# Kernel optimization log

Measured on AMD Instinct MI355X. Metric: run time of the kernel, lower is better.

## Reference

```python
import jax, jax.numpy as jnp
import numpy as np
from functools import partial

ALPHA = 0.1
THETA = 0.5
N_NODES = 100000
N_EDGES = 3200000


def _gcn_norm(edge_index, num_nodes):
    # add self loops, compute symmetric normalization D^-1/2 (A+I) D^-1/2
    loops = jnp.arange(num_nodes, dtype=edge_index.dtype)
    src = jnp.concatenate([edge_index[0], loops])
    dst = jnp.concatenate([edge_index[1], loops])
    deg = jax.ops.segment_sum(jnp.ones_like(dst, dtype=jnp.float32), dst,
                              num_segments=num_nodes)
    dinv = jnp.where(deg > 0, jax.lax.rsqrt(deg), 0.0)
    norm = dinv[src] * dinv[dst]  # [E+N]
    return src, dst, norm


def _propagate(h, src, dst, norm, num_nodes):
    # out[i] = sum_{e: dst[e]=i} norm[e] * h[src[e]]
    msg = h[src] * norm[:, None]
    return jax.ops.segment_sum(msg, dst, num_segments=num_nodes)


def setup_inputs() -> dict:
    key = jax.random.key(0)
    ks = jax.random.split(key, 7)
    H, Fin, Fout, L = 256, 512, 64, 8
    x = jax.random.normal(ks[0], (N_NODES, Fin), dtype=jnp.float32)
    edge_index = jax.random.randint(ks[1], (2, N_EDGES), 0, N_NODES, dtype=jnp.int64)
    s = 1.0 / np.sqrt(Fin)
    W0 = jax.random.normal(ks[2], (Fin, H), dtype=jnp.float32) * s
    b0 = jax.random.normal(ks[3], (H,), dtype=jnp.float32) * 0.01
    Ws = jax.random.normal(ks[4], (L, H, H), dtype=jnp.float32) / np.sqrt(H)
    Wc = jax.random.normal(ks[5], (H, Fout), dtype=jnp.float32) / np.sqrt(H)
    bc = jax.random.normal(ks[6], (Fout,), dtype=jnp.float32) * 0.01
    return {"x": x, "edge_index": edge_index, "W0": W0, "b0": b0,
            "Ws": Ws, "Wc": Wc, "bc": bc}


def reference(x, edge_index, W0, b0, Ws, Wc, bc):
    num_nodes = x.shape[0]
    src, dst, norm = _gcn_norm(edge_index, num_nodes)
    # initial projection (dropout is identity in eval mode)
    x0 = jax.nn.relu(x @ W0 + b0)  # [N, H]
    h = x0
    layer_num = Ws.shape[0]
    for i in range(layer_num):
        beta = float(np.log(THETA / (i + 1) + 1.0))
        agg = _propagate(h, src, dst, norm, num_nodes)          # Ahat @ h
        z = (1.0 - ALPHA) * agg + ALPHA * x0                    # initial residual
        h = jax.nn.relu((1.0 - beta) * z + beta * (z @ Ws[i]))  # identity mapping
    embedding = h
    logits = embedding @ Wc + bc
    soft_label = jax.nn.softmax(logits, axis=1)
    hard_label = jnp.argmax(soft_label, axis=1)
    return logits, embedding, soft_label, hard_label
```

## Files before the change

kernel.cpp:

```cpp
#include <hip/hip_runtime.h>
#include <hip/hip_bf16.h>
#include <math.h>

#define NN   100000
#define FIN  512
#define HH   256
#define FOUT 64

typedef __attribute__((ext_vector_type(8))) short s16x8;
typedef __attribute__((ext_vector_type(4))) float f32x4;

__global__ void k_count(const int* __restrict__ dst, int* __restrict__ cnt, int E) {
    int i = blockIdx.x * 256 + threadIdx.x;
    if (i < E) atomicAdd(&cnt[dst[i]], 1);
}

__global__ void k_block_sums(const int* __restrict__ cnt, int* __restrict__ partial, int n) {
    __shared__ int red[256];
    int base = blockIdx.x * 1024;
    int t = threadIdx.x;
    int s = 0;
#pragma unroll
    for (int i = 0; i < 4; i++) { int idx = base + t * 4 + i; if (idx < n) s += cnt[idx]; }
    red[t] = s; __syncthreads();
    for (int off = 128; off > 0; off >>= 1) {
        if (t < off) red[t] += red[t + off];
        __syncthreads();
    }
    if (t == 0) partial[blockIdx.x] = red[0];
}

__global__ void k_scan_partials(int* partial, int nb, int* row_ptr, int n) {
    if (threadIdx.x == 0) {
        int run = 0;
        for (int i = 0; i < nb; i++) { int v = partial[i]; partial[i] = run; run += v; }
        row_ptr[n] = run;
    }
}

__global__ void k_write_rowptr(const int* __restrict__ cnt, const int* __restrict__ partial,
                               int* __restrict__ row_ptr, int* __restrict__ cur, int n) {
    __shared__ int sc[256];
    int base = blockIdx.x * 1024;
    int t = threadIdx.x;
    int v[4]; int s = 0;
#pragma unroll
    for (int i = 0; i < 4; i++) { int idx = base + t * 4 + i; v[i] = (idx < n) ? cnt[idx] : 0; s += v[i]; }
    sc[t] = s; __syncthreads();
    for (int off = 1; off < 256; off <<= 1) {
        int add = (t >= off) ? sc[t - off] : 0;
        __syncthreads();
        sc[t] += add;
        __syncthreads();
    }
    int run = partial[blockIdx.x] + sc[t] - s;
#pragma unroll
    for (int i = 0; i < 4; i++) {
        int idx = base + t * 4 + i;
        if (idx < n) { row_ptr[idx] = run; cur[idx] = run; run += v[i]; }
    }
}

__global__ void k_dinv(const int* __restrict__ cnt, float* __restrict__ dinv, int n) {
    int i = blockIdx.x * 256 + threadIdx.x;
    if (i < n) dinv[i] = 1.0f / sqrtf((float)(cnt[i] + 1));
}

__global__ void k_scatter(const int* __restrict__ src, const int* __restrict__ dst,
                          const float* __restrict__ dinv, int* __restrict__ cur,
                          int* __restrict__ src_sorted, float* __restrict__ norm_sorted, int E) {
    int i = blockIdx.x * 256 + threadIdx.x;
    if (i < E) {
        int s = src[i], d = dst[i];
        int p = atomicAdd(&cur[d], 1);
        src_sorted[p] = s;
        norm_sorted[p] = dinv[s] * dinv[d];
    }
}

__device__ __forceinline__ short f2bf_rn(float f) {
    unsigned b = __float_as_uint(f);
    unsigned r = b + 0x7FFFu + ((b >> 16) & 1u);
    return (short)(r >> 16);
}
__device__ __forceinline__ float bf2f(short h) {
    return __uint_as_float(((unsigned)(unsigned short)h) << 16);
}
__device__ __forceinline__ void split_bf16(float f, short& hi, short& lo) {
    hi = f2bf_rn(f);
    lo = f2bf_rn(f - bf2f(hi));
}

__global__ void k_wprep(const float* __restrict__ W, short* __restrict__ whi,
                        short* __restrict__ wlo, int K) {
    int t = blockIdx.x * 256 + threadIdx.x;
    int total = K * HH / 8;
    if (t >= total) return;
    int colin = t & 15, g = (t >> 4) & 3, nt = (t >> 6) & 15, kt = t >> 10;
    int col = nt * 16 + colin, kb = kt * 32 + g * 8;
    s16x8 h8, l8;
#pragma unroll
    for (int j = 0; j < 8; j++) {
        float f = W[(size_t)(kb + j) * HH + col];
        short h, l; split_bf16(f, h, l);
        h8[j] = h; l8[j] = l;
    }
    *(s16x8*)&whi[(size_t)t * 8] = h8;
    *(s16x8*)&wlo[(size_t)t * 8] = l8;
}

__global__ void k_wprep_all(const float* __restrict__ Ws, short* __restrict__ whi,
                            short* __restrict__ wlo, int L) {
    int t = blockIdx.x * 256 + threadIdx.x;
    const int per = HH * HH / 8;
    if (t >= L * per) return;
    int layer = t / per;
    int tl = t - layer * per;
    float beta = (float)log(0.5 / (layer + 1) + 1.0);
    const float* W = Ws + (size_t)layer * HH * HH;
    int colin = tl & 15, g = (tl >> 4) & 3, nt = (tl >> 6) & 15, kt = tl >> 10;
    int col = nt * 16 + colin, kb = kt * 32 + g * 8;
    s16x8 h8, l8;
#pragma unroll
    for (int j = 0; j < 8; j++) {
        float f = beta * W[(size_t)(kb + j) * HH + col];
        if ((kb + j) == col) f += 1.0f - beta;
        short h, l; split_bf16(f, h, l);
        h8[j] = h; l8[j] = l;
    }
    *(s16x8*)&whi[(size_t)t * 8] = h8;
    *(s16x8*)&wlo[(size_t)t * 8] = l8;
}

__global__ __launch_bounds__(512, 4) void k_gemm0(
    const float* __restrict__ A, const short* __restrict__ Whi, const short* __restrict__ Wlo,
    const float* __restrict__ bias, float* __restrict__ C, int M) {
    __shared__ short As_hi[2][2048];
    __shared__ short As_lo[2][2048];
    int tid = threadIdx.x, lane = tid & 63, wid = tid >> 6;
    int wm = wid >> 2, wn = wid & 3;
    int bm = blockIdx.x * 64;
    int st_row = tid >> 2, st_g = tid & 3;
    int st_cphys = ((st_row & 15) ^ ((st_g & 1) << 2)) + 16 * st_g + 64 * (st_row >> 4);
    const float* st_ap = A + (size_t)(bm + st_row) * FIN + st_g * 8;
    bool st_ok = (tid < 256) && (bm + st_row) < M;
    int fr_g = lane >> 4, fr_r = lane & 15;
    int fr_base = (fr_r ^ ((fr_g & 1) << 2)) + 16 * fr_g;
    int c0 = (fr_base + 64 * (wm * 2 + 0)) * 8;
    int c1 = (fr_base + 64 * (wm * 2 + 1)) * 8;
    int lane_off = fr_g * 16 + fr_r;
    f32x4 acc[2][4] = {};
    f32x4 v0 = {0.f, 0.f, 0.f, 0.f}, v1 = v0, n0 = v0, n1 = v0;
    if (st_ok) { v0 = *(const f32x4*)(st_ap); v1 = *(const f32x4*)(st_ap + 4); }
    for (int kt = 0; kt < FIN / 32; kt++) {
        int buf = kt & 1;
        if (tid < 256) {
            s16x8 h8, l8;
            float fv[8] = {v0.x, v0.y, v0.z, v0.w, v1.x, v1.y, v1.z, v1.w};
#pragma unroll
            for (int j = 0; j < 8; j++) { short hh, ll; split_bf16(fv[j], hh, ll); h8[j] = hh; l8[j] = ll; }
            *(s16x8*)&As_hi[buf][st_cphys * 8] = h8;
            *(s16x8*)&As_lo[buf][st_cphys * 8] = l8;
            if (kt + 1 < FIN / 32 && st_ok) {
                int k0n = (kt + 1) * 32;
                n0 = *(const f32x4*)(st_ap + k0n);
                n1 = *(const f32x4*)(st_ap + k0n + 4);
            }
        }
        __syncthreads();
        s16x8 ah0 = *(const s16x8*)&As_hi[buf][c0], al0 = *(const s16x8*)&As_lo[buf][c0];
        s16x8 ah1 = *(const s16x8*)&As_hi[buf][c1], al1 = *(const s16x8*)&As_lo[buf][c1];
        size_t btile = (size_t)kt * 1024 + (size_t)(wn * 4) * 64;
#pragma unroll
        for (int ct = 0; ct < 4; ct++) {
            s16x8 bh = *(const s16x8*)&Whi[(btile + ct * 64 + lane_off) * 8];
            s16x8 bl = *(const s16x8*)&Wlo[(btile + ct * 64 + lane_off) * 8];
            acc[0][ct] = __builtin_amdgcn_mfma_f32_16x16x32_bf16(ah0, bh, acc[0][ct], 0, 0, 0);
            acc[0][ct] = __builtin_amdgcn_mfma_f32_16x16x32_bf16(al0, bh, acc[0][ct], 0, 0, 0);
            acc[0][ct] = __builtin_amdgcn_mfma_f32_16x16x32_bf16(ah0, bl, acc[0][ct], 0, 0, 0);
            acc[1][ct] = __builtin_amdgcn_mfma_f32_16x16x32_bf16(ah1, bh, acc[1][ct], 0, 0, 0);
            acc[1][ct] = __builtin_amdgcn_mfma_f32_16x16x32_bf16(al1, bh, acc[1][ct], 0, 0, 0);
            acc[1][ct] = __builtin_amdgcn_mfma_f32_16x16x32_bf16(ah1, bl, acc[1][ct], 0, 0, 0);
        }
        v0 = n0; v1 = n1;
        if (kt + 1 < FIN / 32) __syncthreads();
    }
    int rsub = (lane >> 4) * 4, csub = lane & 15;
#pragma unroll
    for (int rt = 0; rt < 2; rt++)
#pragma unroll
        for (int ct = 0; ct < 4; ct++) {
            int col = wn * 64 + ct * 16 + csub;
            int r0 = bm + wm * 32 + rt * 16 + rsub;
#pragma unroll
            for (int reg = 0; reg < 4; reg++) {
                int row = r0 + reg;
                if (row < M) {
                    float o = fmaxf(acc[rt][ct][reg] + bias[col], 0.f);
                    C[(size_t)(col >> 7) * ((size_t)M * 128) + (size_t)row * 128 + (col & 127)] = o;
                }
            }
        }
}

__global__ __launch_bounds__(256) void k_prop(
    const float* __restrict__ hc, const float* __restrict__ x0c,
    const int* __restrict__ row_ptr, const int* __restrict__ src_sorted,
    const float* __restrict__ norm_sorted, const float* __restrict__ dinv,
    float* __restrict__ zc, int M) {
    int wid = threadIdx.x >> 6, lane = threadIdx.x & 63;
    int node = blockIdx.x * 4 + wid;
    if (node >= M) return;
    int slot = lane >> 5, f4 = (lane & 31) * 4;
    int e0 = __builtin_amdgcn_readfirstlane(row_ptr[node]);
    int e1 = __builtin_amdgcn_readfirstlane(row_ptr[node + 1]);
    f32x4 acc = {0.f, 0.f, 0.f, 0.f};
    int e = e0 + slot;
    for (; e + 2 < e1; e += 4) {
        int s0 = src_sorted[e];     float w0 = norm_sorted[e];
        int s1 = src_sorted[e + 2]; float w1 = norm_sorted[e + 2];
        f32x4 v0 = *(const f32x4*)&hc[(size_t)s0 * 128 + f4];
        f32x4 v1 = *(const f32x4*)&hc[(size_t)s1 * 128 + f4];
        acc += w0 * v0 + w1 * v1;
    }
    if (e < e1) {
        int s0 = src_sorted[e]; float w0 = norm_sorted[e];
        acc += w0 * (*(const f32x4*)&hc[(size_t)s0 * 128 + f4]);
    }
#pragma unroll
    for (int c = 0; c < 4; c++) acc[c] += __shfl_xor(acc[c], 32);
    float di = dinv[node], sw = di * di;
    size_t base = (size_t)node * 128 + f4;
    f32x4 hrow = *(const f32x4*)&hc[base];
    f32x4 xv = *(const f32x4*)&x0c[base];
    f32x4 z = 0.9f * (acc + sw * hrow) + 0.1f * xv;
    if (slot == 0) *(f32x4*)&zc[base] = z;
}

__global__ __launch_bounds__(512, 4) void k_mgemm_z(
    const float* __restrict__ Zc, const short* __restrict__ Whi, const short* __restrict__ Wlo,
    float* __restrict__ C, int M, int rowmajor) {
    __shared__ short As_hi[2][2048];
    __shared__ short As_lo[2][2048];
    int tid = threadIdx.x, lane = tid & 63, wid = tid >> 6;
    int wm = wid >> 2, wn = wid & 3;
    int bm = blockIdx.x * 64;
    size_t CS = (size_t)M * 128;
    int st_row = tid >> 2, st_g = tid & 3;
    bool st_ok = (tid < 256) && (bm + st_row) < M;
    int st_cphys = ((st_row & 15) ^ ((st_g & 1) << 2)) + 16 * st_g + 64 * (st_row >> 4);
    int fr_g = lane >> 4, fr_r = lane & 15;
    int fr_base = (fr_r ^ ((fr_g & 1) << 2)) + 16 * fr_g;
    int c0 = (fr_base + 64 * (wm * 2 + 0)) * 8;
    int c1 = (fr_base + 64 * (wm * 2 + 1)) * 8;
    int lane_off = fr_g * 16 + fr_r;
    f32x4 acc[2][4] = {};
    auto zslab = [&](int kt) {
        int k0 = kt * 32;
        return Zc + (size_t)(k0 >> 7) * CS + (size_t)(bm + st_row) * 128 + (k0 & 127) + st_g * 8;
    };
    f32x4 v0 = {0.f, 0.f, 0.f, 0.f}, v1 = v0, n0 = v0, n1 = v0;
    if (st_ok) { const float* zp = zslab(0); v0 = *(const f32x4*)zp; v1 = *(const f32x4*)(zp + 4); }
    for (int kt = 0; kt < 8; kt++) {
        int buf = kt & 1;
        if (tid < 256) {
            s16x8 h8, l8;
            float fv[8] = {v0.x, v0.y, v0.z, v0.w, v1.x, v1.y, v1.z, v1.w};
#pragma unroll
            for (int j = 0; j < 8; j++) { short hh, ll; split_bf16(fv[j], hh, ll); h8[j] = hh; l8[j] = ll; }
            *(s16x8*)&As_hi[buf][st_cphys * 8] = h8;
            *(s16x8*)&As_lo[buf][st_cphys * 8] = l8;
            if (kt + 1 < 8 && st_ok) {
                const float* zp = zslab(kt + 1);
                n0 = *(const f32x4*)zp; n1 = *(const f32x4*)(zp + 4);
            }
        }
        __syncthreads();
        s16x8 ah0 = *(const s16x8*)&As_hi[buf][c0], al0 = *(const s16x8*)&As_lo[buf][c0];
        s16x8 ah1 = *(const s16x8*)&As_hi[buf][c1], al1 = *(const s16x8*)&As_lo[buf][c1];
        size_t btile = (size_t)kt * 1024 + (size_t)(wn * 4) * 64;
#pragma unroll
        for (int ct = 0; ct < 4; ct++) {
            s16x8 bh = *(const s16x8*)&Whi[(btile + ct * 64 + lane_off) * 8];
            s16x8 bl = *(const s16x8*)&Wlo[(btile + ct * 64 + lane_off) * 8];
            acc[0][ct] = __builtin_amdgcn_mfma_f32_16x16x32_bf16(ah0, bh, acc[0][ct], 0, 0, 0);
            acc[0][ct] = __builtin_amdgcn_mfma_f32_16x16x32_bf16(al0, bh, acc[0][ct], 0, 0, 0);
            acc[0][ct] = __builtin_amdgcn_mfma_f32_16x16x32_bf16(ah0, bl, acc[0][ct], 0, 0, 0);
            acc[1][ct] = __builtin_amdgcn_mfma_f32_16x16x32_bf16(ah1, bh, acc[1][ct], 0, 0, 0);
            acc[1][ct] = __builtin_amdgcn_mfma_f32_16x16x32_bf16(al1, bh, acc[1][ct], 0, 0, 0);
            acc[1][ct] = __builtin_amdgcn_mfma_f32_16x16x32_bf16(ah1, bl, acc[1][ct], 0, 0, 0);
        }
        v0 = n0; v1 = n1;
        if (kt + 1 < 8) __syncthreads();
    }
    int rsub = (lane >> 4) * 4, csub = lane & 15;
#pragma unroll
    for (int rt = 0; rt < 2; rt++)
#pragma unroll
        for (int ct = 0; ct < 4; ct++) {
            int col = wn * 64 + ct * 16 + csub;
            int r0 = bm + wm * 32 + rt * 16 + rsub;
#pragma unroll
            for (int reg = 0; reg < 4; reg++) {
                int row = r0 + reg;
                if (row < M) {
                    float o = fmaxf(acc[rt][ct][reg], 0.f);
                    if (rowmajor) C[(size_t)row * HH + col] = o;
                    else C[(size_t)(col >> 7) * CS + (size_t)row * 128 + (col & 127)] = o;
                }
            }
        }
}

__global__ __launch_bounds__(256) void k_final2(
    const float* __restrict__ h, const float* __restrict__ Wc, const float* __restrict__ bc,
    float* __restrict__ logits, float* __restrict__ soft, float* __restrict__ hard, int M) {
    __shared__ float As[16][64];
    __shared__ float Bs[16][64];
    __shared__ float lg[64][64];
    int tid = threadIdx.x;
    int tx = tid & 15, ty = tid >> 4;
    int bm = blockIdx.x * 64;
    int lm = tid >> 2, lk = (tid & 3) * 4;
    int lkb = tid >> 4, lnb = (tid & 15) * 4;
    bool arow_ok = (bm + lm) < M;
    float acc[4][4] = {};
    for (int k0 = 0; k0 < HH; k0 += 16) {
        float4 av = make_float4(0.f, 0.f, 0.f, 0.f);
        if (arow_ok) av = *(const float4*)&h[(size_t)(bm + lm) * HH + k0 + lk];
        As[lk + 0][lm] = av.x; As[lk + 1][lm] = av.y; As[lk + 2][lm] = av.z; As[lk + 3][lm] = av.w;
        *(float4*)&Bs[lkb][lnb] = *(const float4*)&Wc[(size_t)(k0 + lkb) * FOUT + lnb];
        __syncthreads();
#pragma unroll
        for (int k = 0; k < 16; k++) {
            float4 a = *(const float4*)&As[k][ty * 4];
            float4 b = *(const float4*)&Bs[k][tx * 4];
            acc[0][0] += a.x * b.x; acc[0][1] += a.x * b.y; acc[0][2] += a.x * b.z; acc[0][3] += a.x * b.w;
            acc[1][0] += a.y * b.x; acc[1][1] += a.y * b.y; acc[1][2] += a.y * b.z; acc[1][3] += a.y * b.w;
            acc[2][0] += a.z * b.x; acc[2][1] += a.z * b.y; acc[2][2] += a.z * b.z; acc[2][3] += a.z * b.w;
            acc[3][0] += a.w * b.x; acc[3][1] += a.w * b.y; acc[3][2] += a.w * b.z; acc[3][3] += a.w * b.w;
        }
        __syncthreads();
    }
#pragma unroll
    for (int i = 0; i < 4; i++)
        *(float4*)&lg[ty * 4 + i][tx * 4] = make_float4(acc[i][0], acc[i][1], acc[i][2], acc[i][3]);
    __syncthreads();

    int wid = tid >> 6, lane = tid & 63;
    float bv = bc[lane];
    for (int r = wid * 16; r < wid * 16 + 16; r++) {
        int node = bm + r;
        if (node >= M) continue;
        float v = lg[r][lane] + bv;
        float m = v;
        for (int off = 32; off > 0; off >>= 1) m = fmaxf(m, __shfl_xor(m, off));
        float ev = expf(v - m);
        float s = ev;
        for (int off = 32; off > 0; off >>= 1) s += __shfl_xor(s, off);
        float sm = ev / s;
        int idx = lane; float vv = v;
        for (int off = 1; off < 64; off <<= 1) {
            float ov = __shfl_xor(vv, off);
            int oi = __shfl_xor(idx, off);
            if (ov > vv || (ov == vv && oi < idx)) { vv = ov; idx = oi; }
        }
        logits[(size_t)node * FOUT + lane] = v;
        soft[(size_t)node * FOUT + lane] = sm;
        if (lane == 0) hard[node] = (float)idx;
    }
}

extern "C" void kernel_launch(void* const* d_in, const int* in_sizes, int n_in,
                              void* d_out, int out_size, void* d_ws, size_t ws_size,
                              hipStream_t stream) {
    const float* x  = (const float*)d_in[0];
    const int*   ei = (const int*)d_in[1];
    const float* W0 = (const float*)d_in[2];
    const float* b0 = (const float*)d_in[3];
    const float* Ws = (const float*)d_in[4];
    const float* Wc = (const float*)d_in[5];
    const float* bc = (const float*)d_in[6];
    const int E = in_sizes[1] / 2;
    const int N = in_sizes[0] / FIN;
    const int L = in_sizes[4] / (HH * HH);

    float* out    = (float*)d_out;
    float* logits = out;
    float* emb    = out + (size_t)N * FOUT;
    float* soft   = emb + (size_t)N * HH;
    float* hard   = soft + (size_t)N * FOUT;

    char* p = (char*)d_ws;
    size_t off = 0;
    auto alloc = [&](size_t bytes) { void* r = p + off; off += (bytes + 255) & ~(size_t)255; return r; };
    int*   cnt         = (int*)alloc((size_t)N * 4);
    int*   row_ptr     = (int*)alloc((size_t)(N + 1) * 4);
    int*   cur         = (int*)alloc((size_t)N * 4);
    int*   partial     = (int*)alloc(4096 * 4);
    float* dinv        = (float*)alloc((size_t)N * 4);
    int*   src_sorted  = (int*)alloc((size_t)E * 4);
    float* norm_sorted = (float*)alloc((size_t)E * 4);
    float* X0c         = (float*)alloc((size_t)N * HH * 4);
    float* hAc         = (float*)alloc((size_t)N * HH * 4);
    float* hBc         = (float*)alloc((size_t)N * HH * 4);
    short* W0hi        = (short*)alloc((size_t)FIN * HH * 2);
    short* W0lo        = (short*)alloc((size_t)FIN * HH * 2);
    short* Wshi        = (short*)alloc((size_t)L * HH * HH * 2);
    short* Wslo        = (short*)alloc((size_t)L * HH * HH * 2);

    const int* srcp = ei;
    const int* dstp = ei + E;
    const size_t CS = (size_t)N * 128;

    hipMemsetAsync(cnt, 0, (size_t)N * 4, stream);
    k_count<<<(E + 255) / 256, 256, 0, stream>>>(dstp, cnt, E);
    const int nb = (N + 1023) / 1024;
    k_block_sums<<<nb, 256, 0, stream>>>(cnt, partial, N);
    k_scan_partials<<<1, 64, 0, stream>>>(partial, nb, row_ptr, N);
    k_write_rowptr<<<nb, 256, 0, stream>>>(cnt, partial, row_ptr, cur, N);
    k_dinv<<<(N + 255) / 256, 256, 0, stream>>>(cnt, dinv, N);
    k_scatter<<<(E + 255) / 256, 256, 0, stream>>>(srcp, dstp, dinv, cur, src_sorted, norm_sorted, E);

    k_wprep<<<(FIN * HH / 8 + 255) / 256, 256, 0, stream>>>(W0, W0hi, W0lo, FIN);
    k_wprep_all<<<(L * HH * HH / 8 + 255) / 256, 256, 0, stream>>>(Ws, Wshi, Wslo, L);

    const int nblk = (N + 63) / 64;
    const int npb  = (N + 3) / 4;
    k_gemm0<<<nblk, 512, 0, stream>>>(x, W0hi, W0lo, b0, X0c, N);

    const float* hsrc = X0c;
    for (int i = 0; i < L; i++) {
        int last = (i == L - 1);
        float* hdst = last ? emb : ((i & 1) ? hBc : hAc);
        float* zb = last ? hBc : hdst;
        for (int c = 0; c < 2; c++)
            k_prop<<<npb, 256, 0, stream>>>(hsrc + c * CS, X0c + c * CS, row_ptr,
                                            src_sorted, norm_sorted, dinv, zb + c * CS, N);
        k_mgemm_z<<<nblk, 512, 0, stream>>>(zb, Wshi + (size_t)i * HH * HH, Wslo + (size_t)i * HH * HH,
                                            hdst, N, last);
        hsrc = hdst;
    }
    k_final2<<<nblk, 256, 0, stream>>>(emb, Wc, bc, logits, soft, hard, N);
}
```

Baseline: 4.840 ms.

## Emit z as pre-split bf16 hi/lo tiles in GEMM-ready swizzled layout

The propagation kernel now splits z into bf16 hi/lo parts itself and writes them straight into a per-block, per-k-tile image that matches the GEMM's swizzled LDS layout. The GEMM then copies these tiles into shared memory directly, with no fp32 loads or per-element splitting. This is meant to cut the fp32 z traffic (two 16-bit values take the same bytes but need no conversion) and the address math, and it lets the emb buffer double as the ping-pong h buffer. Separately, the dinv computation is folded into the row_ptr kernel, which removes one launch.

After: 4.958 ms. 2.4% more time.

```diff
diff --git a/kernel.cpp b/kernel.cpp
--- a/kernel.cpp
+++ b/kernel.cpp
@@ -8,6 +8,7 @@
 #define FOUT 64
 
 typedef __attribute__((ext_vector_type(8))) short s16x8;
+typedef __attribute__((ext_vector_type(4))) short s16x4;
 typedef __attribute__((ext_vector_type(4))) float f32x4;
 
 __global__ void k_count(const int* __restrict__ dst, int* __restrict__ cnt, int E) {
@@ -39,7 +40,8 @@
 }
 
 __global__ void k_write_rowptr(const int* __restrict__ cnt, const int* __restrict__ partial,
-                               int* __restrict__ row_ptr, int* __restrict__ cur, int n) {
+                               int* __restrict__ row_ptr, int* __restrict__ cur,
+                               float* __restrict__ dinv, int n) {
     __shared__ int sc[256];
     int base = blockIdx.x * 1024;
     int t = threadIdx.x;
@@ -57,13 +59,11 @@
 #pragma unroll
     for (int i = 0; i < 4; i++) {
         int idx = base + t * 4 + i;
-        if (idx < n) { row_ptr[idx] = run; cur[idx] = run; run += v[i]; }
-    }
-}
-
-__global__ void k_dinv(const int* __restrict__ cnt, float* __restrict__ dinv, int n) {
-    int i = blockIdx.x * 256 + threadIdx.x;
-    if (i < n) dinv[i] = 1.0f / sqrtf((float)(cnt[i] + 1));
+        if (idx < n) {
+            row_ptr[idx] = run; cur[idx] = run; run += v[i];
+            dinv[idx] = 1.0f / sqrtf((float)(v[i] + 1));
+        }
+    }
 }
 
 __global__ void k_scatter(const int* __restrict__ src, const int* __restrict__ dst,
@@ -207,7 +207,7 @@
     const float* __restrict__ hc, const float* __restrict__ x0c,
     const int* __restrict__ row_ptr, const int* __restrict__ src_sorted,
     const float* __restrict__ norm_sorted, const float* __restrict__ dinv,
-    float* __restrict__ zc, int M) {
+    short* __restrict__ zT, int M, int chunk) {
     int wid = threadIdx.x >> 6, lane = threadIdx.x & 63;
     int node = blockIdx.x * 4 + wid;
     if (node >= M) return;
@@ -234,45 +234,55 @@
     f32x4 hrow = *(const f32x4*)&hc[base];
     f32x4 xv = *(const f32x4*)&x0c[base];
     f32x4 z = 0.9f * (acc + sw * hrow) + 0.1f * xv;
-    if (slot == 0) *(f32x4*)&zc[base] = z;
+    if (slot == 0) {
+        s16x4 zh, zl;
+        { short h, l; split_bf16(z.x, h, l); zh[0] = h; zl[0] = l; }
+        { short h, l; split_bf16(z.y, h, l); zh[1] = h; zl[1] = l; }
+        { short h, l; split_bf16(z.z, h, l); zh[2] = h; zl[2] = l; }
+        { short h, l; split_bf16(z.w, h, l); zh[3] = h; zl[3] = l; }
+        int kt_loc = ((chunk << 7) + f4) >> 5;
+        int g = (f4 >> 3) & 3;
+        int j = f4 & 7;
+        int rl = node & 63, blk = node >> 6;
+        int cphys = ((rl & 15) ^ ((g & 1) << 2)) + 16 * g + 64 * (rl >> 4);
+        size_t zi = ((size_t)(blk * 8 + kt_loc) * 2) * 2048 + (size_t)cphys * 8 + j;
+        *(s16x4*)&zT[zi] = zh;
+        *(s16x4*)&zT[zi + 2048] = zl;
+    }
 }
 
 __global__ __launch_bounds__(512, 4) void k_mgemm_z(
-    const float* __restrict__ Zc, const short* __restrict__ Whi, const short* __restrict__ Wlo,
+    const short* __restrict__ zT, const short* __restrict__ Whi, const short* __restrict__ Wlo,
     float* __restrict__ C, int M, int rowmajor) {
     __shared__ short As_hi[2][2048];
     __shared__ short As_lo[2][2048];
     int tid = threadIdx.x, lane = tid & 63, wid = tid >> 6;
     int wm = wid >> 2, wn = wid & 3;
-    int bm = blockIdx.x * 64;
+    int blk = blockIdx.x;
+    int bm = blk * 64;
     size_t CS = (size_t)M * 128;
-    int st_row = tid >> 2, st_g = tid & 3;
-    bool st_ok = (tid < 256) && (bm + st_row) < M;
-    int st_cphys = ((st_row & 15) ^ ((st_g & 1) << 2)) + 16 * st_g + 64 * (st_row >> 4);
     int fr_g = lane >> 4, fr_r = lane & 15;
     int fr_base = (fr_r ^ ((fr_g & 1) << 2)) + 16 * fr_g;
     int c0 = (fr_base + 64 * (wm * 2 + 0)) * 8;
     int c1 = (fr_base + 64 * (wm * 2 + 1)) * 8;
     int lane_off = fr_g * 16 + fr_r;
     f32x4 acc[2][4] = {};
-    auto zslab = [&](int kt) {
-        int k0 = kt * 32;
-        return Zc + (size_t)(k0 >> 7) * CS + (size_t)(bm + st_row) * 128 + (k0 & 127) + st_g * 8;
-    };
-    f32x4 v0 = {0.f, 0.f, 0.f, 0.f}, v1 = v0, n0 = v0, n1 = v0;
-    if (st_ok) { const float* zp = zslab(0); v0 = *(const f32x4*)zp; v1 = *(const f32x4*)(zp + 4); }
+    auto img = [&](int kt) { return zT + ((size_t)(blk * 8 + kt) * 2) * 2048; };
+    s16x8 vh = {}, vl = {}, nh = {}, nl = {};
+    if (tid < 256) {
+        const short* pi = img(0);
+        vh = *(const s16x8*)&pi[tid * 8];
+        vl = *(const s16x8*)&pi[2048 + tid * 8];
+    }
     for (int kt = 0; kt < 8; kt++) {
         int buf = kt & 1;
         if (tid < 256) {
-            s16x8 h8, l8;
-            float fv[8] = {v0.x, v0.y, v0.z, v0.w, v1.x, v1.y, v1.z, v1.w};
-#pragma unroll
-            for (int j = 0; j < 8; j++) { short hh, ll; split_bf16(fv[j], hh, ll); h8[j] = hh; l8[j] = ll; }
-            *(s16x8*)&As_hi[buf][st_cphys * 8] = h8;
-            *(s16x8*)&As_lo[buf][st_cphys * 8] = l8;
-            if (kt + 1 < 8 && st_ok) {
-                const float* zp = zslab(kt + 1);
-                n0 = *(const f32x4*)zp; n1 = *(const f32x4*)(zp + 4);
+            *(s16x8*)&As_hi[buf][tid * 8] = vh;
+            *(s16x8*)&As_lo[buf][tid * 8] = vl;
+            if (kt + 1 < 8) {
+                const short* pi = img(kt + 1);
+                nh = *(const s16x8*)&pi[tid * 8];
+                nl = *(const s16x8*)&pi[2048 + tid * 8];
             }
         }
         __syncthreads();
@@ -290,7 +300,7 @@
             acc[1][ct] = __builtin_amdgcn_mfma_f32_16x16x32_bf16(al1, bh, acc[1][ct], 0, 0, 0);
             acc[1][ct] = __builtin_amdgcn_mfma_f32_16x16x32_bf16(ah1, bl, acc[1][ct], 0, 0, 0);
         }
-        v0 = n0; v1 = n1;
+        vh = nh; vl = nl;
         if (kt + 1 < 8) __syncthreads();
     }
     int rsub = (lane >> 4) * 4, csub = lane & 15;
@@ -391,6 +401,8 @@
     float* soft   = emb + (size_t)N * HH;
     float* hard   = soft + (size_t)N * FOUT;
 
+    const int nblk = (N + 63) / 64;
+
     char* p = (char*)d_ws;
     size_t off = 0;
     auto alloc = [&](size_t bytes) { void* r = p + off; off += (bytes + 255) & ~(size_t)255; return r; };
@@ -403,7 +415,7 @@
     float* norm_sorted = (float*)alloc((size_t)E * 4);
     float* X0c         = (float*)alloc((size_t)N * HH * 4);
     float* hAc         = (float*)alloc((size_t)N * HH * 4);
-    float* hBc         = (float*)alloc((size_t)N * HH * 4);
+    short* zT          = (short*)alloc((size_t)nblk * 8 * 2 * 2048 * 2);
     short* W0hi        = (short*)alloc((size_t)FIN * HH * 2);
     short* W0lo        = (short*)alloc((size_t)FIN * HH * 2);
     short* Wshi        = (short*)alloc((size_t)L * HH * HH * 2);
@@ -418,26 +430,23 @@
     const int nb = (N + 1023) / 1024;
     k_block_sums<<<nb, 256, 0, stream>>>(cnt, partial, N);
     k_scan_partials<<<1, 64, 0, stream>>>(partial, nb, row_ptr, N);
-    k_write_rowptr<<<nb, 256, 0, stream>>>(cnt, partial, row_ptr, cur, N);
-    k_dinv<<<(N + 255) / 256, 256, 0, stream>>>(cnt, dinv, N);
+    k_write_rowptr<<<nb, 256, 0, stream>>>(cnt, partial, row_ptr, cur, dinv, N);
     k_scatter<<<(E + 255) / 256, 256, 0, stream>>>(srcp, dstp, dinv, cur, src_sorted, norm_sorted, E);
 
     k_wprep<<<(FIN * HH / 8 + 255) / 256, 256, 0, stream>>>(W0, W0hi, W0lo, FIN);
     k_wprep_all<<<(L * HH * HH / 8 + 255) / 256, 256, 0, stream>>>(Ws, Wshi, Wslo, L);
 
-    const int nblk = (N + 63) / 64;
-    const int npb  = (N + 3) / 4;
+    const int npb = (N + 3) / 4;
     k_gemm0<<<nblk, 512, 0, stream>>>(x, W0hi, W0lo, b0, X0c, N);
 
     const float* hsrc = X0c;
     for (int i = 0; i < L; i++) {
         int last = (i == L - 1);
-        float* hdst = last ? emb : ((i & 1) ? hBc : hAc);
-        float* zb = last ? hBc : hdst;
+        float* hdst = last ? emb : ((i & 1) ? emb : hAc);
         for (int c = 0; c < 2; c++)
             k_prop<<<npb, 256, 0, stream>>>(hsrc + c * CS, X0c + c * CS, row_ptr,
-                                            src_sorted, norm_sorted, dinv, zb + c * CS, N);
-        k_mgemm_z<<<nblk, 512, 0, stream>>>(zb, Wshi + (size_t)i * HH * HH, Wslo + (size_t)i * HH * HH,
+                                            src_sorted, norm_sorted, dinv, zT, N, c);
+        k_mgemm_z<<<nblk, 512, 0, stream>>>(zT, Wshi + (size_t)i * HH * HH, Wslo + (size_t)i * HH * HH,
                                             hdst, N, last);
         hsrc = hdst;
     }
```
